# Performance work log

Hardware: AMD Instinct MI355X
Metric: run time of the kernel (lower is better)

## Reference

```python
import jax, jax.numpy as jnp
import numpy as np


def setup_inputs() -> dict:
    key = jax.random.key(0)
    k1, k2, k3 = jax.random.split(key, 3)
    B, H, L, OUT = 4096, 2048, 8, 1024
    x = jax.random.normal(k1, (B, H), dtype=jnp.float32)
    W = jax.random.normal(k2, (L, H, H), dtype=jnp.float32)
    beta = jax.random.normal(k3, (H, OUT), dtype=jnp.float32)
    return {"x": x, "W": W, "beta": beta}


def _fcn_forward(x, W, beta):
    h = W.shape[-1]
    scale = 1.0 / jnp.sqrt(jnp.asarray(h, x.dtype))
    # Linear1d: (x[:,None]*W).sum(-1)/sqrt(h) == x @ W.T / sqrt(h); then ReLU.
    def layer(y, Wi):
        y = jax.nn.relu(jnp.einsum('bi,oi->bo', y, Wi) * scale)
        return y, None
    y, _ = jax.lax.scan(layer, x, W)
    # readout: y @ beta / h
    return jnp.einsum('bh,ho->bo', y, beta) / h


def reference(x, W, beta):
    return _fcn_forward(x, W, beta)
```

## Files before the change

### kernel.cpp

```cpp
#include <hip/hip_runtime.h>
#include <cstdint>
#include <cstddef>

typedef __bf16          bf16x8  __attribute__((ext_vector_type(8)));
typedef float           f32x4   __attribute__((ext_vector_type(4)));
typedef unsigned short  u16x8   __attribute__((ext_vector_type(8)));

__device__ __forceinline__ unsigned short f32_bf16_rne(float f) {
  union { float f; unsigned u; } v; v.f = f;
  unsigned u = v.u + 0x7FFFu + ((v.u >> 16) & 1u);
  return (unsigned short)(u >> 16);
}

__global__ void cvt_f32_bf16(const float* __restrict__ in,
                             unsigned short* __restrict__ out, int n8) {
  int idx = blockIdx.x * 256 + threadIdx.x;
  int stride = gridDim.x * 256;
  for (int i = idx; i < n8; i += stride) {
    float4 a = ((const float4*)in)[2 * (size_t)i];
    float4 b = ((const float4*)in)[2 * (size_t)i + 1];
    u16x8 o;
    o[0] = f32_bf16_rne(a.x); o[1] = f32_bf16_rne(a.y);
    o[2] = f32_bf16_rne(a.z); o[3] = f32_bf16_rne(a.w);
    o[4] = f32_bf16_rne(b.x); o[5] = f32_bf16_rne(b.y);
    o[6] = f32_bf16_rne(b.z); o[7] = f32_bf16_rne(b.w);
    *(u16x8*)(out + (size_t)i * 8) = o;
  }
}

__global__ void cvt_transpose(const float* __restrict__ in,
                              unsigned short* __restrict__ out, int H, int O) {
  __shared__ float tile[32][33];
  int o0 = blockIdx.x * 32, h0 = blockIdx.y * 32;
  int tx = threadIdx.x & 31, ty = threadIdx.x >> 5;
  #pragma unroll
  for (int i = ty; i < 32; i += 8)
    tile[i][tx] = in[(size_t)(h0 + i) * O + (o0 + tx)];
  __syncthreads();
  #pragma unroll
  for (int i = ty; i < 32; i += 8)
    out[(size_t)(o0 + i) * H + (h0 + tx)] = f32_bf16_rne(tile[tx][i]);
}

#define GLOAD(gp, lp)                                                   \
  __builtin_amdgcn_global_load_lds(                                     \
      (const __attribute__((address_space(1))) void*)(gp),              \
      (__attribute__((address_space(3))) void*)(lp), 16, 0, 0)

#define MFMA16 __builtin_amdgcn_mfma_f32_16x16x32_bf16

__device__ __forceinline__ void read_frags(bf16x8 (&fa)[2][4], bf16x8 (&fb)[2][4],
                                           const __bf16* sa, const __bf16* sb,
                                           int aBase, int bBase, int cc0, int cc1) {
  #pragma unroll
  for (int kk = 0; kk < 2; ++kk) {
    const int c = kk ? cc1 : cc0;
    #pragma unroll
    for (int m = 0; m < 4; ++m)
      fa[kk][m] = *(const bf16x8*)(sa + aBase + m * 1024 + c);
    #pragma unroll
    for (int n = 0; n < 4; ++n)
      fb[kk][n] = *(const bf16x8*)(sb + bBase + n * 1024 + c);
  }
}

__device__ __forceinline__ void mfma32(f32x4 (&acc)[4][4],
                                       const bf16x8 (&fa)[2][4],
                                       const bf16x8 (&fb)[2][4]) {
  #pragma unroll
  for (int kk = 0; kk < 2; ++kk)
    #pragma unroll
    for (int m = 0; m < 4; ++m)
      #pragma unroll
      for (int n = 0; n < 4; ++n)
        acc[m][n] = MFMA16(fa[kk][m], fb[kk][n], acc[m][n], 0, 0, 0);
}


#define BODY(T, FA_C, FB_C, FA_N, FB_N)                                   \
  do {                                                                    \
    const int t_ = (T);                                                   \
    if (t_ + 2 < NT) {                                                    \
      const size_t ko = (size_t)(t_ + 2) * 64;                            \
      __bf16* dA = As + sst * 8192;                                       \
      __bf16* dB = Bs + sst * 16384;                                      \
      GLOAD(gA0 + ko, dA + 0 * 4096 + tid * 8);                           \
      GLOAD(gA1 + ko, dA + 1 * 4096 + tid * 8);                           \
      GLOAD(gB0 + ko, dB + 0 * 4096 + tid * 8);                           \
      GLOAD(gB1 + ko, dB + 1 * 4096 + tid * 8);                           \
      GLOAD(gB2 + ko, dB + 2 * 4096 + tid * 8);                           \
      GLOAD(gB3 + ko, dB + 3 * 4096 + tid * 8);                           \
      asm volatile("s_waitcnt lgkmcnt(0)" ::: "memory");                  \
      asm volatile("s_waitcnt vmcnt(6)" ::: "memory");                    \
    } else {                                                              \
      asm volatile("s_waitcnt lgkmcnt(0)" ::: "memory");                  \
      asm volatile("s_waitcnt vmcnt(0)" ::: "memory");                    \
    }                                                                     \
    __builtin_amdgcn_s_barrier();                                         \
    __builtin_amdgcn_sched_barrier(0);                                    \
    if (t_ + 1 < NT)                                                      \
      read_frags(FA_N, FB_N, As + srd * 8192, Bs + srd * 16384,           \
                 aBase, bBase, cc0, cc1);                                 \
    __builtin_amdgcn_s_setprio(1);                                        \
    mfma32(acc, FA_C, FB_C);                                              \
    __builtin_amdgcn_s_setprio(0);                                        \
    sst = sst + 1; if (sst == 3) sst = 0;                                 \
    srd = srd + 1; if (srd == 3) srd = 0;                                 \
  } while (0)

__global__ __launch_bounds__(512, 2)
void gemm128x256p(const unsigned short* __restrict__ A,
                  const unsigned short* __restrict__ B,
                  unsigned short* __restrict__ Cp, int N, int K, float scale) {
  __shared__ __bf16 As[3 * 128 * 64] __attribute__((aligned(16)));
  __shared__ __bf16 Bs[3 * 256 * 64] __attribute__((aligned(16)));

  const int tid  = threadIdx.x;
  const int lane = tid & 63;
  const int wave = tid >> 6;
  const int wr   = wave >> 2;
  const int wc   = wave & 3;
  const int l16  = lane & 15;
  const int kgrp = lane >> 4;

  const int brow0 = blockIdx.y * 128;
  const int bcol0 = blockIdx.x * 256;

  const int xorv  = (l16 & 7) << 3;
  const int cc0   = (kgrp * 8) ^ xorv;
  const int cc1   = (32 + kgrp * 8) ^ xorv;
  const int aBase = (wr * 64 + l16) * 64;
  const int bBase = (wc * 64 + l16) * 64;

  const int srow = tid >> 3;
  const int scol = ((tid & 7) * 8) ^ ((srow & 7) << 3);
  const unsigned short* gA0 = A + (size_t)(brow0 +   0 + srow) * K + scol;
  const unsigned short* gA1 = A + (size_t)(brow0 +  64 + srow) * K + scol;
  const unsigned short* gB0 = B + (size_t)(bcol0 +   0 + srow) * K + scol;
  const unsigned short* gB1 = B + (size_t)(bcol0 +  64 + srow) * K + scol;
  const unsigned short* gB2 = B + (size_t)(bcol0 + 128 + srow) * K + scol;
  const unsigned short* gB3 = B + (size_t)(bcol0 + 192 + srow) * K + scol;

  f32x4  acc[4][4] = {};
  bf16x8 fa0[2][4], fb0[2][4], fa1[2][4], fb1[2][4];

  const int NT = K >> 6;

  {
    GLOAD(gA0, &As[0 * 4096 + tid * 8]);
    GLOAD(gA1, &As[1 * 4096 + tid * 8]);
    GLOAD(gB0, &Bs[0 * 4096 + tid * 8]);
    GLOAD(gB1, &Bs[1 * 4096 + tid * 8]);
    GLOAD(gB2, &Bs[2 * 4096 + tid * 8]);
    GLOAD(gB3, &Bs[3 * 4096 + tid * 8]);
    GLOAD(gA0 + 64, &As[8192 + 0 * 4096 + tid * 8]);
    GLOAD(gA1 + 64, &As[8192 + 1 * 4096 + tid * 8]);
    GLOAD(gB0 + 64, &Bs[16384 + 0 * 4096 + tid * 8]);
    GLOAD(gB1 + 64, &Bs[16384 + 1 * 4096 + tid * 8]);
    GLOAD(gB2 + 64, &Bs[16384 + 2 * 4096 + tid * 8]);
    GLOAD(gB3 + 64, &Bs[16384 + 3 * 4096 + tid * 8]);
    asm volatile("s_waitcnt vmcnt(6)" ::: "memory");
    __builtin_amdgcn_s_barrier();
    read_frags(fa0, fb0, As, Bs, aBase, bBase, cc0, cc1);
  }

  int sst = 2, srd = 1;
  for (int t = 0; t < NT; t += 2) {
    BODY(t,     fa0, fb0, fa1, fb1);
    BODY(t + 1, fa1, fb1, fa0, fb0);
  }

  const int crow0 = brow0 + wr * 64 + kgrp * 4;
  const int ccol0 = bcol0 + wc * 64 + l16;
  #pragma unroll
  for (int m = 0; m < 4; ++m)
    #pragma unroll
    for (int n = 0; n < 4; ++n)
      #pragma unroll
      for (int j = 0; j < 4; ++j) {
        float v = acc[m][n][j] * scale;
        v = v > 0.0f ? v : 0.0f;
        Cp[(size_t)(crow0 + m * 16 + j) * N + (ccol0 + n * 16)] = f32_bf16_rne(v);
      }
}

__global__ __launch_bounds__(256)
void gemm_bt_f32(const unsigned short* __restrict__ A,
                 const unsigned short* __restrict__ B,
                 float* __restrict__ C, int N, int K, float scale) {
  __shared__ __bf16 As[128 * 32] __attribute__((aligned(16)));
  __shared__ __bf16 Bs[128 * 32] __attribute__((aligned(16)));

  const int tid  = threadIdx.x;
  const int lane = tid & 63;
  const int wave = tid >> 6;
  const int wr   = wave >> 1, wc = wave & 1;
  const int l16  = lane & 15, kgrp = lane >> 4;

  const int brow0 = blockIdx.y * 128;
  const int bcol0 = blockIdx.x * 128;

  const int offb  = wave * 2048 + lane * 16;
  const int srow  = offb >> 6;
  const int selem = (offb & 63) >> 1;
  const unsigned short* gA0 = A + (size_t)(brow0 + srow) * K + selem;
  const unsigned short* gA1 = A + (size_t)(brow0 + srow + 16) * K + selem;
  const unsigned short* gB0 = B + (size_t)(bcol0 + srow) * K + selem;
  const unsigned short* gB1 = B + (size_t)(bcol0 + srow + 16) * K + selem;
  __bf16* lA0 = &As[wave * 1024];
  __bf16* lA1 = &As[wave * 1024 + 512];
  __bf16* lB0 = &Bs[wave * 1024];
  __bf16* lB1 = &Bs[wave * 1024 + 512];

  f32x4 acc[4][4] = {};
  const int aoff = (wr * 64 + l16) * 32 + kgrp * 8;
  const int boff = (wc * 64 + l16) * 32 + kgrp * 8;

  for (int k0 = 0; k0 < K; k0 += 32) {
    GLOAD(gA0 + k0, lA0);
    GLOAD(gA1 + k0, lA1);
    GLOAD(gB0 + k0, lB0);
    GLOAD(gB1 + k0, lB1);
    asm volatile("s_waitcnt vmcnt(0)" ::: "memory");
    __syncthreads();

    bf16x8 af[4], bfv[4];
    #pragma unroll
    for (int m = 0; m < 4; ++m)
      af[m] = *(const bf16x8*)(As + aoff + m * 16 * 32);
    #pragma unroll
    for (int n = 0; n < 4; ++n)
      bfv[n] = *(const bf16x8*)(Bs + boff + n * 16 * 32);
    #pragma unroll
    for (int m = 0; m < 4; ++m)
      #pragma unroll
      for (int n = 0; n < 4; ++n)
        acc[m][n] = MFMA16(af[m], bfv[n], acc[m][n], 0, 0, 0);
    __syncthreads();
  }

  const int crow0 = brow0 + wr * 64 + kgrp * 4;
  const int ccol0 = bcol0 + wc * 64 + l16;
  #pragma unroll
  for (int m = 0; m < 4; ++m)
    #pragma unroll
    for (int n = 0; n < 4; ++n)
      #pragma unroll
      for (int j = 0; j < 4; ++j)
        C[(size_t)(crow0 + m * 16 + j) * N + (ccol0 + n * 16)] =
            acc[m][n][j] * scale;
}

extern "C" void kernel_launch(void* const* d_in, const int* in_sizes, int n_in,
                              void* d_out, int out_size, void* d_ws, size_t ws_size,
                              hipStream_t stream) {
  const float* x    = (const float*)d_in[0];
  const float* W    = (const float*)d_in[1];
  const float* beta = (const float*)d_in[2];
  float* out = (float*)d_out;

  const int Bn = 4096, H = 2048, L = 8, O = 1024;

  unsigned short* y0    = (unsigned short*)d_ws;
  unsigned short* y1    = y0 + (size_t)Bn * H;
  unsigned short* Wb    = y1 + (size_t)Bn * H;
  unsigned short* betaT = Wb + (size_t)L * H * H;

  {
    int n8 = L * H * H / 8;
    cvt_f32_bf16<<<2048, 256, 0, stream>>>(W, Wb, n8);
  }
  {
    int n8 = Bn * H / 8;
    int grid = (n8 + 255) / 256;
    if (grid > 2048) grid = 2048;
    cvt_f32_bf16<<<grid, 256, 0, stream>>>(x, y0, n8);
  }
  cvt_transpose<<<dim3(O / 32, H / 32), 256, 0, stream>>>(beta, betaT, H, O);

  const float s1 = 0.02209708691207961f;
  unsigned short* yin = y0;
  unsigned short* yout = y1;
  for (int l = 0; l < L; ++l) {
    gemm128x256p<<<dim3(H / 256, Bn / 128), 512, 0, stream>>>(
        yin, Wb + (size_t)l * H * H, yout, H, H, s1);
    unsigned short* t = yin; yin = yout; yout = t;
  }
  gemm_bt_f32<<<dim3(O / 128, Bn / 128), 256, 0, stream>>>(yin, betaT, out, O, H,
                                                           1.0f / 2048.0f);
}
```

Baseline: 404.6 us.

## Restructure GEMM main loop into two half-K phases with split global loads

Replaces the register double-buffered fragment pipeline with a per-K-tile loop split into two 32-wide phases. Each phase reads its fragments from LDS, issues half of the next tile's global-to-LDS loads, synchronizes with barriers, then runs 16 MFMAs. This halves fragment register pressure and spreads the global load issue across the tile, in exchange for more barriers per iteration and less overlap between LDS reads and MFMA execution.

```diff
diff --git a/kernel.cpp b/kernel.cpp
--- a/kernel.cpp
+++ b/kernel.cpp
@@ -49,69 +49,11 @@
 
 #define MFMA16 __builtin_amdgcn_mfma_f32_16x16x32_bf16
 
-__device__ __forceinline__ void read_frags(bf16x8 (&fa)[2][4], bf16x8 (&fb)[2][4],
-                                           const __bf16* sa, const __bf16* sb,
-                                           int aBase, int bBase, int cc0, int cc1) {
-  #pragma unroll
-  for (int kk = 0; kk < 2; ++kk) {
-    const int c = kk ? cc1 : cc0;
-    #pragma unroll
-    for (int m = 0; m < 4; ++m)
-      fa[kk][m] = *(const bf16x8*)(sa + aBase + m * 1024 + c);
-    #pragma unroll
-    for (int n = 0; n < 4; ++n)
-      fb[kk][n] = *(const bf16x8*)(sb + bBase + n * 1024 + c);
-  }
-}
-
-__device__ __forceinline__ void mfma32(f32x4 (&acc)[4][4],
-                                       const bf16x8 (&fa)[2][4],
-                                       const bf16x8 (&fb)[2][4]) {
-  #pragma unroll
-  for (int kk = 0; kk < 2; ++kk)
-    #pragma unroll
-    for (int m = 0; m < 4; ++m)
-      #pragma unroll
-      for (int n = 0; n < 4; ++n)
-        acc[m][n] = MFMA16(fa[kk][m], fb[kk][n], acc[m][n], 0, 0, 0);
-}
-
-
-#define BODY(T, FA_C, FB_C, FA_N, FB_N)                                   \
-  do {                                                                    \
-    const int t_ = (T);                                                   \
-    if (t_ + 2 < NT) {                                                    \
-      const size_t ko = (size_t)(t_ + 2) * 64;                            \
-      __bf16* dA = As + sst * 8192;                                       \
-      __bf16* dB = Bs + sst * 16384;                                      \
-      GLOAD(gA0 + ko, dA + 0 * 4096 + tid * 8);                           \
-      GLOAD(gA1 + ko, dA + 1 * 4096 + tid * 8);                           \
-      GLOAD(gB0 + ko, dB + 0 * 4096 + tid * 8);                           \
-      GLOAD(gB1 + ko, dB + 1 * 4096 + tid * 8);                           \
-      GLOAD(gB2 + ko, dB + 2 * 4096 + tid * 8);                           \
-      GLOAD(gB3 + ko, dB + 3 * 4096 + tid * 8);                           \
-      asm volatile("s_waitcnt lgkmcnt(0)" ::: "memory");                  \
-      asm volatile("s_waitcnt vmcnt(6)" ::: "memory");                    \
-    } else {                                                              \
-      asm volatile("s_waitcnt lgkmcnt(0)" ::: "memory");                  \
-      asm volatile("s_waitcnt vmcnt(0)" ::: "memory");                    \
-    }                                                                     \
-    __builtin_amdgcn_s_barrier();                                         \
-    __builtin_amdgcn_sched_barrier(0);                                    \
-    if (t_ + 1 < NT)                                                      \
-      read_frags(FA_N, FB_N, As + srd * 8192, Bs + srd * 16384,           \
-                 aBase, bBase, cc0, cc1);                                 \
-    __builtin_amdgcn_s_setprio(1);                                        \
-    mfma32(acc, FA_C, FB_C);                                              \
-    __builtin_amdgcn_s_setprio(0);                                        \
-    sst = sst + 1; if (sst == 3) sst = 0;                                 \
-    srd = srd + 1; if (srd == 3) srd = 0;                                 \
-  } while (0)
 
 __global__ __launch_bounds__(512, 2)
-void gemm128x256p(const unsigned short* __restrict__ A,
-                  const unsigned short* __restrict__ B,
-                  unsigned short* __restrict__ Cp, int N, int K, float scale) {
+void gemm8p(const unsigned short* __restrict__ A,
+            const unsigned short* __restrict__ B,
+            unsigned short* __restrict__ Cp, int N, int K, float scale) {
   __shared__ __bf16 As[3 * 128 * 64] __attribute__((aligned(16)));
   __shared__ __bf16 Bs[3 * 256 * 64] __attribute__((aligned(16)));
 
@@ -141,8 +83,7 @@
   const unsigned short* gB2 = B + (size_t)(bcol0 + 128 + srow) * K + scol;
   const unsigned short* gB3 = B + (size_t)(bcol0 + 192 + srow) * K + scol;
 
-  f32x4  acc[4][4] = {};
-  bf16x8 fa0[2][4], fb0[2][4], fa1[2][4], fb1[2][4];
+  f32x4 acc[4][4] = {};
 
   const int NT = K >> 6;
 
@@ -161,13 +102,79 @@
     GLOAD(gB3 + 64, &Bs[16384 + 3 * 4096 + tid * 8]);
     asm volatile("s_waitcnt vmcnt(6)" ::: "memory");
     __builtin_amdgcn_s_barrier();
-    read_frags(fa0, fb0, As, Bs, aBase, bBase, cc0, cc1);
-  }
-
-  int sst = 2, srd = 1;
-  for (int t = 0; t < NT; t += 2) {
-    BODY(t,     fa0, fb0, fa1, fb1);
-    BODY(t + 1, fa1, fb1, fa0, fb0);
+    __builtin_amdgcn_sched_barrier(0);
+  }
+
+  int srd = 0, sst = 2;
+  for (int t = 0; t < NT; ++t) {
+    const __bf16* rA = As + srd * 8192;
+    const __bf16* rB = Bs + srd * 16384;
+    __bf16* dA = As + sst * 8192;
+    __bf16* dB = Bs + sst * 16384;
+    const bool stg = (t + 2 < NT);
+    const size_t ko = (size_t)(t + 2) * 64;
+
+    {
+      bf16x8 fa[4], fb[4];
+      #pragma unroll
+      for (int m = 0; m < 4; ++m)
+        fa[m] = *(const bf16x8*)(rA + aBase + m * 1024 + cc0);
+      #pragma unroll
+      for (int n = 0; n < 4; ++n)
+        fb[n] = *(const bf16x8*)(rB + bBase + n * 1024 + cc0);
+      if (stg) {
+        GLOAD(gA0 + ko, dA + 0 * 4096 + tid * 8);
+        GLOAD(gA1 + ko, dA + 1 * 4096 + tid * 8);
+        GLOAD(gB0 + ko, dB + 0 * 4096 + tid * 8);
+      }
+      __builtin_amdgcn_sched_barrier(0);
+      __builtin_amdgcn_s_barrier();
+      asm volatile("s_waitcnt lgkmcnt(0)" ::: "memory");
+      __builtin_amdgcn_sched_barrier(0);
+      __builtin_amdgcn_s_setprio(1);
+      #pragma unroll
+      for (int m = 0; m < 4; ++m)
+        #pragma unroll
+        for (int n = 0; n < 4; ++n)
+          acc[m][n] = MFMA16(fa[m], fb[n], acc[m][n], 0, 0, 0);
+      __builtin_amdgcn_s_setprio(0);
+      __builtin_amdgcn_sched_barrier(0);
+      __builtin_amdgcn_s_barrier();
+    }
+
+    {
+      bf16x8 fa[4], fb[4];
+      #pragma unroll
+      for (int m = 0; m < 4; ++m)
+        fa[m] = *(const bf16x8*)(rA + aBase + m * 1024 + cc1);
+      #pragma unroll
+      for (int n = 0; n < 4; ++n)
+        fb[n] = *(const bf16x8*)(rB + bBase + n * 1024 + cc1);
+      if (stg) {
+        GLOAD(gB1 + ko, dB + 1 * 4096 + tid * 8);
+        GLOAD(gB2 + ko, dB + 2 * 4096 + tid * 8);
+        GLOAD(gB3 + ko, dB + 3 * 4096 + tid * 8);
+        asm volatile("s_waitcnt vmcnt(6)" ::: "memory");
+      } else if (t == NT - 2) {
+        asm volatile("s_waitcnt vmcnt(0)" ::: "memory");
+      }
+      __builtin_amdgcn_sched_barrier(0);
+      __builtin_amdgcn_s_barrier();
+      asm volatile("s_waitcnt lgkmcnt(0)" ::: "memory");
+      __builtin_amdgcn_sched_barrier(0);
+      __builtin_amdgcn_s_setprio(1);
+      #pragma unroll
+      for (int m = 0; m < 4; ++m)
+        #pragma unroll
+        for (int n = 0; n < 4; ++n)
+          acc[m][n] = MFMA16(fa[m], fb[n], acc[m][n], 0, 0, 0);
+      __builtin_amdgcn_s_setprio(0);
+      __builtin_amdgcn_sched_barrier(0);
+      __builtin_amdgcn_s_barrier();
+    }
+
+    srd = srd + 1 == 3 ? 0 : srd + 1;
+    sst = sst + 1 == 3 ? 0 : sst + 1;
   }
 
   const int crow0 = brow0 + wr * 64 + kgrp * 4;
@@ -282,7 +289,7 @@
   unsigned short* yin = y0;
   unsigned short* yout = y1;
   for (int l = 0; l < L; ++l) {
-    gemm128x256p<<<dim3(H / 256, Bn / 128), 512, 0, stream>>>(
+    gemm8p<<<dim3(H / 256, Bn / 128), 512, 0, stream>>>(
         yin, Wb + (size_t)l * H * H, yout, H, H, s1);
     unsigned short* t = yin; yin = yout; yout = t;
   }
```

Result: no change. 408.2 us (+0.9%).

## Fuse next-layer weight conversion into GEMM and split K-step into half-phases

Applied to the files above, without the earlier changes.

The up-front conversion of all eight fp32 weight layers to bf16 is replaced: only layer 0 is converted up front, and each layer's GEMM converts the next layer's weights inside its main loop, so that memory-bound work overlaps MFMA compute. The GEMM loop is also restructured: fragments are no longer double-buffered in registers. Each 64-wide K tile is split into two 32-wide phases, each doing its own LDS reads, issuing part of the global prefetch, then a barrier and 16 MFMAs. This lowers register pressure but doubles the barriers per K tile and exposes LDS read latency. The added global traffic inside the GEMM may also contend with operand loads.

```diff
diff --git a/kernel.cpp b/kernel.cpp
--- a/kernel.cpp
+++ b/kernel.cpp
@@ -5,6 +5,7 @@
 typedef __bf16          bf16x8  __attribute__((ext_vector_type(8)));
 typedef float           f32x4   __attribute__((ext_vector_type(4)));
 typedef unsigned short  u16x8   __attribute__((ext_vector_type(8)));
+typedef unsigned short  u16x4   __attribute__((ext_vector_type(4)));
 
 __device__ __forceinline__ unsigned short f32_bf16_rne(float f) {
   union { float f; unsigned u; } v; v.f = f;
@@ -49,69 +50,91 @@
 
 #define MFMA16 __builtin_amdgcn_mfma_f32_16x16x32_bf16
 
-__device__ __forceinline__ void read_frags(bf16x8 (&fa)[2][4], bf16x8 (&fb)[2][4],
-                                           const __bf16* sa, const __bf16* sb,
-                                           int aBase, int bBase, int cc0, int cc1) {
-  #pragma unroll
-  for (int kk = 0; kk < 2; ++kk) {
-    const int c = kk ? cc1 : cc0;
-    #pragma unroll
-    for (int m = 0; m < 4; ++m)
-      fa[kk][m] = *(const bf16x8*)(sa + aBase + m * 1024 + c);
-    #pragma unroll
-    for (int n = 0; n < 4; ++n)
-      fb[kk][n] = *(const bf16x8*)(sb + bBase + n * 1024 + c);
-  }
-}
-
-__device__ __forceinline__ void mfma32(f32x4 (&acc)[4][4],
-                                       const bf16x8 (&fa)[2][4],
-                                       const bf16x8 (&fb)[2][4]) {
-  #pragma unroll
-  for (int kk = 0; kk < 2; ++kk)
-    #pragma unroll
-    for (int m = 0; m < 4; ++m)
-      #pragma unroll
-      for (int n = 0; n < 4; ++n)
-        acc[m][n] = MFMA16(fa[kk][m], fb[kk][n], acc[m][n], 0, 0, 0);
-}
-
-
-#define BODY(T, FA_C, FB_C, FA_N, FB_N)                                   \
-  do {                                                                    \
-    const int t_ = (T);                                                   \
-    if (t_ + 2 < NT) {                                                    \
-      const size_t ko = (size_t)(t_ + 2) * 64;                            \
-      __bf16* dA = As + sst * 8192;                                       \
-      __bf16* dB = Bs + sst * 16384;                                      \
-      GLOAD(gA0 + ko, dA + 0 * 4096 + tid * 8);                           \
-      GLOAD(gA1 + ko, dA + 1 * 4096 + tid * 8);                           \
-      GLOAD(gB0 + ko, dB + 0 * 4096 + tid * 8);                           \
-      GLOAD(gB1 + ko, dB + 1 * 4096 + tid * 8);                           \
-      GLOAD(gB2 + ko, dB + 2 * 4096 + tid * 8);                           \
-      GLOAD(gB3 + ko, dB + 3 * 4096 + tid * 8);                           \
-      asm volatile("s_waitcnt lgkmcnt(0)" ::: "memory");                  \
-      asm volatile("s_waitcnt vmcnt(6)" ::: "memory");                    \
-    } else {                                                              \
-      asm volatile("s_waitcnt lgkmcnt(0)" ::: "memory");                  \
-      asm volatile("s_waitcnt vmcnt(0)" ::: "memory");                    \
-    }                                                                     \
-    __builtin_amdgcn_s_barrier();                                         \
-    __builtin_amdgcn_sched_barrier(0);                                    \
-    if (t_ + 1 < NT)                                                      \
-      read_frags(FA_N, FB_N, As + srd * 8192, Bs + srd * 16384,           \
-                 aBase, bBase, cc0, cc1);                                 \
-    __builtin_amdgcn_s_setprio(1);                                        \
-    mfma32(acc, FA_C, FB_C);                                              \
-    __builtin_amdgcn_s_setprio(0);                                        \
-    sst = sst + 1; if (sst == 3) sst = 0;                                 \
-    srd = srd + 1; if (srd == 3) srd = 0;                                 \
+
+#define BODYP(T, CVL, CVS)                                                    \
+  do {                                                                        \
+    const int t_ = (T);                                                       \
+    const __bf16* rA = As + srd * 8192;                                       \
+    const __bf16* rB = Bs + srd * 16384;                                      \
+    __bf16* dA = As + sst * 8192;                                             \
+    __bf16* dB = Bs + sst * 16384;                                            \
+    const bool stg = (t_ + 2 < NT);                                           \
+    const size_t ko = (size_t)(t_ + 2) * 64;                                  \
+    {                                                  \
+      bf16x8 fa[4], fb[4];                                                    \
+      _Pragma("unroll")                                                       \
+      for (int m = 0; m < 4; ++m)                                             \
+        fa[m] = *(const bf16x8*)(rA + aBase + m * 1024 + cc0);                \
+      _Pragma("unroll")                                                       \
+      for (int n = 0; n < 4; ++n)                                             \
+        fb[n] = *(const bf16x8*)(rB + bBase + n * 1024 + cc0);                \
+      if (stg) {                                                              \
+        GLOAD(gA0 + ko, dA + 0 * 4096 + tid * 8);                             \
+        GLOAD(gA1 + ko, dA + 1 * 4096 + tid * 8);                             \
+        GLOAD(gB0 + ko, dB + 0 * 4096 + tid * 8);                             \
+      }                                                                       \
+      if (docv && t_ < 8)                                                     \
+        CVL = *(const f32x4*)(Wn + (((size_t)(bid * 8 + t_)) * 512 + tid) * 4);\
+      if (docv && t_ >= 1 && t_ <= 8) {                                       \
+        u16x4 o;                                                              \
+        o[0] = f32_bf16_rne(CVS[0]); o[1] = f32_bf16_rne(CVS[1]);             \
+        o[2] = f32_bf16_rne(CVS[2]); o[3] = f32_bf16_rne(CVS[3]);             \
+        *(u16x4*)(Wbn + (((size_t)(bid * 8 + (t_ - 1))) * 512 + tid) * 4) = o;\
+      }                                                                       \
+      __builtin_amdgcn_sched_barrier(0);                                      \
+      __builtin_amdgcn_s_barrier();                                           \
+      asm volatile("s_waitcnt lgkmcnt(0)" ::: "memory");                      \
+      __builtin_amdgcn_sched_barrier(0);                                      \
+      __builtin_amdgcn_s_setprio(1);                                          \
+      _Pragma("unroll")                                                       \
+      for (int m = 0; m < 4; ++m)                                             \
+        _Pragma("unroll")                                                     \
+        for (int n = 0; n < 4; ++n)                                           \
+          acc[m][n] = MFMA16(fa[m], fb[n], acc[m][n], 0, 0, 0);               \
+      __builtin_amdgcn_s_setprio(0);                                          \
+      __builtin_amdgcn_sched_barrier(0);                                      \
+      __builtin_amdgcn_s_barrier();                                           \
+    }                                                                         \
+    {                                                  \
+      bf16x8 fa[4], fb[4];                                                    \
+      _Pragma("unroll")                                                       \
+      for (int m = 0; m < 4; ++m)                                             \
+        fa[m] = *(const bf16x8*)(rA + aBase + m * 1024 + cc1);                \
+      _Pragma("unroll")                                                       \
+      for (int n = 0; n < 4; ++n)                                             \
+        fb[n] = *(const bf16x8*)(rB + bBase + n * 1024 + cc1);                \
+      if (stg) {                                                              \
+        GLOAD(gB1 + ko, dB + 1 * 4096 + tid * 8);                             \
+        GLOAD(gB2 + ko, dB + 2 * 4096 + tid * 8);                             \
+        GLOAD(gB3 + ko, dB + 3 * 4096 + tid * 8);                             \
+        asm volatile("s_waitcnt vmcnt(6)" ::: "memory");                      \
+      } else if (t_ == NT - 2) {                                              \
+        asm volatile("s_waitcnt vmcnt(0)" ::: "memory");                      \
+      }                                                                       \
+      __builtin_amdgcn_sched_barrier(0);                                      \
+      __builtin_amdgcn_s_barrier();                                           \
+      asm volatile("s_waitcnt lgkmcnt(0)" ::: "memory");                      \
+      __builtin_amdgcn_sched_barrier(0);                                      \
+      __builtin_amdgcn_s_setprio(1);                                          \
+      _Pragma("unroll")                                                       \
+      for (int m = 0; m < 4; ++m)                                             \
+        _Pragma("unroll")                                                     \
+        for (int n = 0; n < 4; ++n)                                           \
+          acc[m][n] = MFMA16(fa[m], fb[n], acc[m][n], 0, 0, 0);               \
+      __builtin_amdgcn_s_setprio(0);                                          \
+      __builtin_amdgcn_sched_barrier(0);                                      \
+      __builtin_amdgcn_s_barrier();                                           \
+    }                                                                         \
+    srd = srd + 1 == 3 ? 0 : srd + 1;                                         \
+    sst = sst + 1 == 3 ? 0 : sst + 1;                                         \
   } while (0)
 
 __global__ __launch_bounds__(512, 2)
-void gemm128x256p(const unsigned short* __restrict__ A,
-                  const unsigned short* __restrict__ B,
-                  unsigned short* __restrict__ Cp, int N, int K, float scale) {
+void gemm8p(const unsigned short* __restrict__ A,
+            const unsigned short* __restrict__ B,
+            unsigned short* __restrict__ Cp, int N, int K, float scale,
+            const float* __restrict__ Wn, unsigned short* __restrict__ Wbn,
+            int docv) {
   __shared__ __bf16 As[3 * 128 * 64] __attribute__((aligned(16)));
   __shared__ __bf16 Bs[3 * 256 * 64] __attribute__((aligned(16)));
 
@@ -125,6 +148,7 @@
 
   const int brow0 = blockIdx.y * 128;
   const int bcol0 = blockIdx.x * 256;
+  const int bid   = blockIdx.y * 8 + blockIdx.x;
 
   const int xorv  = (l16 & 7) << 3;
   const int cc0   = (kgrp * 8) ^ xorv;
@@ -141,8 +165,8 @@
   const unsigned short* gB2 = B + (size_t)(bcol0 + 128 + srow) * K + scol;
   const unsigned short* gB3 = B + (size_t)(bcol0 + 192 + srow) * K + scol;
 
-  f32x4  acc[4][4] = {};
-  bf16x8 fa0[2][4], fb0[2][4], fa1[2][4], fb1[2][4];
+  f32x4 acc[4][4] = {};
+  f32x4 cvE = {}, cvO = {};
 
   const int NT = K >> 6;
 
@@ -161,13 +185,13 @@
     GLOAD(gB3 + 64, &Bs[16384 + 3 * 4096 + tid * 8]);
     asm volatile("s_waitcnt vmcnt(6)" ::: "memory");
     __builtin_amdgcn_s_barrier();
-    read_frags(fa0, fb0, As, Bs, aBase, bBase, cc0, cc1);
-  }
-
-  int sst = 2, srd = 1;
+    __builtin_amdgcn_sched_barrier(0);
+  }
+
+  int srd = 0, sst = 2;
   for (int t = 0; t < NT; t += 2) {
-    BODY(t,     fa0, fb0, fa1, fb1);
-    BODY(t + 1, fa1, fb1, fa0, fb0);
+    BODYP(t,     cvE, cvO);
+    BODYP(t + 1, cvO, cvE);
   }
 
   const int crow0 = brow0 + wr * 64 + kgrp * 4;
@@ -266,10 +290,7 @@
   unsigned short* Wb    = y1 + (size_t)Bn * H;
   unsigned short* betaT = Wb + (size_t)L * H * H;
 
-  {
-    int n8 = L * H * H / 8;
-    cvt_f32_bf16<<<2048, 256, 0, stream>>>(W, Wb, n8);
-  }
+  cvt_f32_bf16<<<2048, 256, 0, stream>>>(W, Wb, H * H / 8);
   {
     int n8 = Bn * H / 8;
     int grid = (n8 + 255) / 256;
@@ -282,8 +303,12 @@
   unsigned short* yin = y0;
   unsigned short* yout = y1;
   for (int l = 0; l < L; ++l) {
-    gemm128x256p<<<dim3(H / 256, Bn / 128), 512, 0, stream>>>(
-        yin, Wb + (size_t)l * H * H, yout, H, H, s1);
+    const bool hasNext = (l + 1 < L);
+    const float* Wn = hasNext ? W + (size_t)(l + 1) * H * H : W;
+    unsigned short* Wbn = hasNext ? Wb + (size_t)(l + 1) * H * H : Wb;
+    gemm8p<<<dim3(H / 256, Bn / 128), 512, 0, stream>>>(
+        yin, Wb + (size_t)l * H * H, yout, H, H, s1,
+        Wn, Wbn, hasNext ? 1 : 0);
     unsigned short* t = yin; yin = yout; yout = t;
   }
   gemm_bt_f32<<<dim3(O / 128, Bn / 128), 256, 0, stream>>>(yin, betaT, out, O, H,
```

Measured after the change: 423.8 us. +4.8%, slower.
